# Kernel tuning notes

Measured on AMD Instinct MI355X. Metric: run time of the kernel, lower is better.

Reference implementation:

```python
import jax, jax.numpy as jnp
import numpy as np

D_MODEL = 1024
N_HEADS = 16
MIXTURE_FACTOR = 4
LATENT = D_MODEL // MIXTURE_FACTOR  # 256
D_K = D_MODEL // N_HEADS            # 64
B, L = 2, 2048


def setup_inputs() -> dict:
    key = jax.random.key(0)
    ks = jax.random.split(key, 13)
    s_in = 1.0 / np.sqrt(D_MODEL)
    s_lat = 1.0 / np.sqrt(LATENT)
    return {
        "queries": jax.random.normal(ks[0], (B, L, 1, D_MODEL), jnp.float32),
        "keys": jax.random.normal(ks[1], (B, L, 1, D_MODEL), jnp.float32),
        "values": jax.random.normal(ks[2], (B, L, 1, D_MODEL), jnp.float32),
        "Wq": jax.random.normal(ks[3], (D_MODEL, D_MODEL), jnp.float32) * s_in,
        "bq": jnp.zeros((D_MODEL,), jnp.float32),
        "Wd": jax.random.normal(ks[4], (D_MODEL, LATENT), jnp.float32) * s_in,
        "bd": jnp.zeros((LATENT,), jnp.float32),
        "Wk": jax.random.normal(ks[5], (LATENT, D_MODEL), jnp.float32) * s_lat,
        "bk": jnp.zeros((D_MODEL,), jnp.float32),
        "Wv": jax.random.normal(ks[6], (LATENT, D_MODEL), jnp.float32) * s_lat,
        "bv": jnp.zeros((D_MODEL,), jnp.float32),
        "Wo": jax.random.normal(ks[7], (D_MODEL, D_MODEL), jnp.float32) * s_in,
        "bo": jnp.zeros((D_MODEL,), jnp.float32),
    }


def reference(queries, keys, values, Wq, bq, Wd, bd, Wk, bk, Wv, bv, Wo, bo):
    b, l, h_in, e = queries.shape  # h_in == 1, e == d_model
    s = keys.shape[1]
    scale = D_K ** -0.5

    q_flat = queries.reshape(b, l, e)
    Q = (q_flat @ Wq + bq).reshape(b, l, N_HEADS, D_K)

    kv_input = keys.reshape(b, s, e)
    latent = kv_input @ Wd + bd                      # [b, s, latent]
    K = (latent @ Wk + bk).reshape(b, s, N_HEADS, D_K)
    V = (latent @ Wv + bv).reshape(b, s, N_HEADS, D_K)

    scores = jnp.einsum('blhe,bshe->bhls', Q, K) * scale  # [b, h, l, s]
    causal = jnp.triu(jnp.ones((l, s), dtype=bool), k=1)
    scores = jnp.where(causal, -jnp.inf, scores)
    A = jax.nn.softmax(scores, axis=-1)

    out = jnp.einsum('bhls,bshd->blhd', A, V).reshape(b, l, N_HEADS * D_K)
    return out @ Wo + bo
```

## Files before the change

### kernel.cpp

```cpp
#include <hip/hip_runtime.h>
#include <stdint.h>


#define DM 1024
#define NH 16
#define DK 64
#define LL 2048

typedef float  f32x4  __attribute__((ext_vector_type(4)));
typedef __bf16 bf16x8 __attribute__((ext_vector_type(8)));
typedef short  s16x8  __attribute__((ext_vector_type(8)));

__device__ __forceinline__ unsigned short f2bf(float f) {
    union { float f; unsigned int u; } v; v.f = f;
    return (unsigned short)((v.u + 0x7fffu + ((v.u >> 16) & 1u)) >> 16);
}
__device__ __forceinline__ unsigned int pack2(float a, float b) {
    return (unsigned int)f2bf(a) | ((unsigned int)f2bf(b) << 16);
}
__device__ __forceinline__ bf16x8 ld8(const unsigned short* p) {
    s16x8 s = *(const s16x8*)p;
    return __builtin_bit_cast(bf16x8, s);
}
__device__ __forceinline__ void gl16(const void* g, void* l) {
    __builtin_amdgcn_global_load_lds((__attribute__((address_space(1))) void*)(g),
                                     (__attribute__((address_space(3))) void*)(l),
                                     16, 0, 0);
}

__global__ __launch_bounds__(256)
void prep_k(const float* __restrict__ Wq, const float* __restrict__ Wd,
            const float* __restrict__ Wk, const float* __restrict__ Wv,
            const float* __restrict__ Wo, const float* __restrict__ queries,
            const float* __restrict__ keys,
            unsigned short* __restrict__ WqT, unsigned short* __restrict__ WdT,
            unsigned short* __restrict__ WkvT, unsigned short* __restrict__ WoT,
            unsigned short* __restrict__ Qb, unsigned short* __restrict__ Kb) {
    int bid = blockIdx.x;
    const int t = threadIdx.x;

    const float* W; unsigned short* WT; int TK, TN;
    if (bid < 1024)      { W = Wq; WT = WqT;  TK = 1024; TN = 1024; }
    else if (bid < 1280) { bid -= 1024; W = Wd; WT = WdT; TK = 1024; TN = 256; }
    else if (bid < 1536) { bid -= 1280; W = Wk; WT = WkvT; TK = 256; TN = 1024; }
    else if (bid < 1792) { bid -= 1536; W = Wv; WT = WkvT + (size_t)1024 * 256; TK = 256; TN = 1024; }
    else if (bid < 2816) { bid -= 1792; W = Wo; WT = WoT;  TK = 1024; TN = 1024; }
    else {
        bid -= 2816;
        const float* src; unsigned short* dst;
        if (bid < 1024) { src = queries; dst = Qb; }
        else            { bid -= 1024; src = keys; dst = Kb; }
        const size_t base = (size_t)bid * 4096;
#pragma unroll
        for (int i = 0; i < 4; ++i) {
            float4 f = *(const float4*)(src + base + (size_t)(i * 256 + t) * 4);
            uint2 u = { pack2(f.x, f.y), pack2(f.z, f.w) };
            *(uint2*)(dst + base + (size_t)(i * 256 + t) * 4) = u;
        }
        return;
    }
    __shared__ float tile[32][33];
    const int tx = t & 31, ty = t >> 5;
    const int bx = bid % (TK / 32), by = bid / (TK / 32);
    const int k0 = bx * 32, n0 = by * 32;
#pragma unroll
    for (int i = 0; i < 4; ++i)
        tile[ty + 8 * i][tx] = W[(size_t)(k0 + ty + 8 * i) * TN + n0 + tx];
    __syncthreads();
#pragma unroll
    for (int i = 0; i < 4; ++i)
        WT[(size_t)(n0 + ty + 8 * i) * TK + k0 + tx] = f2bf(tile[tx][ty + 8 * i]);
}

__device__ __forceinline__ void stage6(const unsigned short* gA, const unsigned short* gB,
                                       int kk, int K,
                                       unsigned short* lA, unsigned short* lB) {
#pragma unroll
    for (int s = 0; s < 4; ++s) gl16(gA + kk + (size_t)s * 8 * K, lA + s * 512);
#pragma unroll
    for (int s = 0; s < 2; ++s) gl16(gB + kk + (size_t)s * 8 * K, lB + s * 512);
}

__device__ __forceinline__ void mfma16(const unsigned short* As, const unsigned short* Bs,
                                       const int aoff[4][2], const int boff[2][2],
                                       f32x4 acc[4][2]) {
#pragma unroll
    for (int ks = 0; ks < 2; ++ks) {
        bf16x8 a[4], b[2];
#pragma unroll
        for (int i = 0; i < 4; ++i) a[i] = ld8(As + aoff[i][ks]);
#pragma unroll
        for (int j = 0; j < 2; ++j) b[j] = ld8(Bs + boff[j][ks]);
#pragma unroll
        for (int i = 0; i < 4; ++i)
#pragma unroll
            for (int j = 0; j < 2; ++j)
                acc[i][j] = __builtin_amdgcn_mfma_f32_16x16x32_bf16(a[i], b[j], acc[i][j], 0, 0, 0);
    }
}

template<int MODE>
__global__ __launch_bounds__(256)
void gemm_k(const unsigned short* __restrict__ Ap, const unsigned short* __restrict__ Bt,
            const float* __restrict__ bias, void* __restrict__ Cp,
            const unsigned short* __restrict__ Ap2, const unsigned short* __restrict__ Bt2,
            const float* __restrict__ bias2, void* __restrict__ Cp2,
            int K) {
    __shared__ unsigned short Sh0[12288];
    __shared__ unsigned short Sh1[12288];

    int bid = blockIdx.x;
    const unsigned short* A;
    const unsigned short* B;
    const float* bs;
    bool second = false;
    int m0, n0;
    if (MODE == 0 && bid >= 512) {
        bid -= 512; A = Ap2; B = Bt2; bs = bias2; second = true;
        const int xcd = bid & 7, s = bid >> 3;
        n0 = (s & 3) * 64; m0 = (xcd * 4 + (s >> 2)) * 128;
    } else {
        A = Ap; B = Bt; bs = bias;
        const int xcd = bid & 7, s = bid >> 3;
        if (MODE == 2) { n0 = (s & 31) * 64; m0 = (xcd * 4 + (s >> 5)) * 128; }
        else           { n0 = (s & 15) * 64; m0 = (xcd * 4 + (s >> 4)) * 128; }
    }

    const int t = threadIdx.x, lane = t & 63, wv = t >> 6;
    const int quad = lane >> 4, l15 = lane & 15;

    const int lr8 = lane >> 3;
    const int g8 = (lane & 7) ^ (lr8 & 7);
    const unsigned short* gA = A + (size_t)(m0 + wv * 32 + lr8) * K + g8 * 8;
    const unsigned short* gB = B + (size_t)(n0 + wv * 16 + lr8) * K + g8 * 8;
    unsigned short* lA0 = Sh0 + wv * 2048;
    unsigned short* lB0 = Sh0 + 8192 + wv * 1024;
    unsigned short* lA1 = Sh1 + wv * 2048;
    unsigned short* lB1 = Sh1 + 8192 + wv * 1024;

    int aoff[4][2], boff[2][2];
#pragma unroll
    for (int i = 0; i < 4; ++i) {
        const int ra = (wv >> 1) * 64 + i * 16 + l15;
#pragma unroll
        for (int ks = 0; ks < 2; ++ks)
            aoff[i][ks] = ra * 64 + (((ks * 4 + quad) ^ (ra & 7)) << 3);
    }
#pragma unroll
    for (int j = 0; j < 2; ++j) {
        const int rb = (wv & 1) * 32 + j * 16 + l15;
#pragma unroll
        for (int ks = 0; ks < 2; ++ks)
            boff[j][ks] = rb * 64 + (((ks * 4 + quad) ^ (rb & 7)) << 3);
    }

    f32x4 acc[4][2] = {};
    const int niter = K >> 6;

    stage6(gA, gB, 0, K, lA0, lB0);
    __syncthreads();
    for (int it = 0; it < niter; it += 2) {
        const int kk = it << 6;
        if (it + 1 < niter) stage6(gA, gB, kk + 64, K, lA1, lB1);
        mfma16(Sh0, Sh0 + 8192, aoff, boff, acc);
        __syncthreads();
        if (it + 1 < niter) {
            if (it + 2 < niter) stage6(gA, gB, kk + 128, K, lA0, lB0);
            mfma16(Sh1, Sh1 + 8192, aoff, boff, acc);
            __syncthreads();
        }
    }

    const bool isV = (MODE == 2) && (n0 >= 1024);
    if (!isV) {
#pragma unroll
        for (int j = 0; j < 2; ++j) {
            const int col = n0 + (wv & 1) * 32 + j * 16 + l15;
            const float bvv = bs[col];
#pragma unroll
            for (int i = 0; i < 4; ++i) {
                const int rowb = m0 + (wv >> 1) * 64 + i * 16 + quad * 4;
#pragma unroll
                for (int r = 0; r < 4; ++r) {
                    const float v = acc[i][j][r] + bvv;
                    const int row = rowb + r;
                    if (MODE == 1)
                        ((float*)Cp)[(size_t)row * 1024 + col] = v;
                    else if (second)
                        ((unsigned short*)Cp2)[(size_t)row * 256 + col] = f2bf(v);
                    else
                        ((unsigned short*)Cp)[(size_t)row * 1024 + col] = f2bf(v);
                }
            }
        }
    } else {
        unsigned short* Ld = Sh0;
#pragma unroll
        for (int j = 0; j < 2; ++j) {
            const int dloc = (wv & 1) * 32 + j * 16 + l15;
            const float bvv = bias2[(n0 - 1024) + dloc];
#pragma unroll
            for (int i = 0; i < 4; ++i) {
                const int tokb = (wv >> 1) * 64 + i * 16 + quad * 4;
#pragma unroll
                for (int r = 0; r < 4; ++r)
                    Ld[dloc * 136 + tokb + r] = f2bf(acc[i][j][r] + bvv);
            }
        }
        __syncthreads();
        const int dloc = t >> 2;
        const int tk0 = (t & 3) * 32;
        const int bb = m0 >> 11;
        unsigned short* dst = (unsigned short*)Cp2 +
            ((size_t)bb * 1024 + (n0 - 1024) + dloc) * LL + (m0 & (LL - 1)) + tk0;
        const unsigned short* srcp = Ld + dloc * 136 + tk0;
#pragma unroll
        for (int c = 0; c < 4; ++c)
            *(uint4*)(dst + c * 8) = *(const uint4*)(srcp + c * 8);
    }
}

__global__ __launch_bounds__(512)
void attn6_k(const unsigned short* __restrict__ Qp,
             const unsigned short* __restrict__ Kp,
             const unsigned short* __restrict__ VpT,
             unsigned short* __restrict__ Op) {
    __shared__ unsigned short Ks[2][4096];
    __shared__ unsigned short Vs[2][4096];
    __shared__ unsigned short Ps[8][16][72];

    const int t = threadIdx.x, lane = t & 63, wv = t >> 6;
    const int grp = wv >> 2, w4 = wv & 3;
    const int quad = lane >> 4, l15 = lane & 15;

    const int bid = blockIdx.x;
    const int xcd = bid & 7, s = bid >> 3;
    const int pair = s & 15;
    const int combo = xcd * 4 + (s >> 4);
    const int h = combo & 15, b = combo >> 4;

    const int srow = w4 * 16 + (lane >> 3);
    const int g8 = (lane & 7) ^ ((lane >> 3) & 7);
    unsigned short* lK = &Ks[grp][w4 * 1024];
    unsigned short* lV = &Vs[grp][w4 * 1024];
    const int sw = l15 & 7;
    float* cb = (float*)&Ks[0][0];

    for (int tsel = 0; tsel < 2; ++tsel) {
        const int tile = tsel ? (31 - pair) : pair;
        const int q0 = tile * 64;

        const unsigned short* qp = Qp + (size_t)(b * LL + q0 + w4 * 16 + l15) * DM + h * DK;
        const bf16x8 aq0 = ld8(qp + quad * 8);
        const bf16x8 aq1 = ld8(qp + 32 + quad * 8);

        f32x4 acc[4] = {};
        float lrow[4] = {0.f, 0.f, 0.f, 0.f};
        const int rowq = q0 + w4 * 16 + quad * 4;

        const int nit = tile / 2 + 1;
        for (int it = 0; it < nit; ++it) {
            const int c = 2 * it + grp;
            const bool active = (c <= tile);
            const int kt = c * 64;
            __syncthreads();
            if (active) {
                const unsigned short* kg = Kp + (size_t)(b * LL + kt + srow) * DM + h * DK + g8 * 8;
                const unsigned short* vg = VpT + ((size_t)(b * NH + h) * DK + srow) * LL + kt + g8 * 8;
                gl16(kg, lK);             gl16(kg + (size_t)8 * DM, lK + 512);
                gl16(vg, lV);             gl16(vg + (size_t)8 * LL, lV + 512);
            }
            __syncthreads();
            if (!active) continue;

            f32x4 s4[4];
#pragma unroll
            for (int sub = 0; sub < 4; ++sub) {
                const int base = (sub * 16 + l15) * 64;
                f32x4 ss = {};
                bf16x8 b0 = ld8(&Ks[grp][base + ((quad ^ sw) << 3)]);
                ss = __builtin_amdgcn_mfma_f32_16x16x32_bf16(aq0, b0, ss, 0, 0, 0);
                bf16x8 b1 = ld8(&Ks[grp][base + (((4 + quad) ^ sw) << 3)]);
                ss = __builtin_amdgcn_mfma_f32_16x16x32_bf16(aq1, b1, ss, 0, 0, 0);
                s4[sub] = ss;
            }

            if (c == tile) {
#pragma unroll
                for (int sub = 0; sub < 4; ++sub) {
                    const int col = kt + sub * 16 + l15;
#pragma unroll
                    for (int r = 0; r < 4; ++r) {
                        float e = exp2f(fmaf(s4[sub][r], 0.18033688011112042f, -16.0f));
                        if (col > rowq + r) e = 0.f;
                        lrow[r] += e;
                        Ps[wv][quad * 4 + r][sub * 16 + l15] =
                            (unsigned short)(__builtin_bit_cast(unsigned int, e) >> 16);
                    }
                }
            } else {
#pragma unroll
                for (int sub = 0; sub < 4; ++sub) {
#pragma unroll
                    for (int r = 0; r < 4; ++r) {
                        float e = exp2f(fmaf(s4[sub][r], 0.18033688011112042f, -16.0f));
                        lrow[r] += e;
                        Ps[wv][quad * 4 + r][sub * 16 + l15] =
                            (unsigned short)(__builtin_bit_cast(unsigned int, e) >> 16);
                    }
                }
            }

#pragma unroll
            for (int ks = 0; ks < 2; ++ks) {
                bf16x8 ap = ld8(&Ps[wv][l15][ks * 32 + quad * 8]);
#pragma unroll
                for (int sub = 0; sub < 4; ++sub) {
                    bf16x8 bv = ld8(&Vs[grp][(sub * 16 + l15) * 64 + (((ks * 4 + quad) ^ sw) << 3)]);
                    acc[sub] = __builtin_amdgcn_mfma_f32_16x16x32_bf16(ap, bv, acc[sub], 0, 0, 0);
                }
            }
        }

        __syncthreads();
        const int base = (w4 * 64 + lane) * 20;
        if (grp == 1) {
#pragma unroll
            for (int sub = 0; sub < 4; ++sub)
#pragma unroll
                for (int r = 0; r < 4; ++r) cb[base + sub * 4 + r] = acc[sub][r];
#pragma unroll
            for (int r = 0; r < 4; ++r) cb[base + 16 + r] = lrow[r];
        }
        __syncthreads();
        if (grp == 0) {
#pragma unroll
            for (int sub = 0; sub < 4; ++sub)
#pragma unroll
                for (int r = 0; r < 4; ++r) acc[sub][r] += cb[base + sub * 4 + r];
#pragma unroll
            for (int r = 0; r < 4; ++r) {
                lrow[r] += cb[base + 16 + r];
#pragma unroll
                for (int off = 1; off < 16; off <<= 1)
                    lrow[r] += __shfl_xor(lrow[r], off, 64);
                lrow[r] = __builtin_amdgcn_rcpf(lrow[r]);
            }
#pragma unroll
            for (int sub = 0; sub < 4; ++sub)
#pragma unroll
                for (int r = 0; r < 4; ++r)
                    Op[(size_t)(b * LL + rowq + r) * DM + h * DK + sub * 16 + l15] =
                        f2bf(acc[sub][r] * lrow[r]);
        }
    }
}

extern "C" void kernel_launch(void* const* d_in, const int* in_sizes, int n_in,
                              void* d_out, int out_size, void* d_ws, size_t ws_size,
                              hipStream_t stream) {
    const float* queries = (const float*)d_in[0];
    const float* keys    = (const float*)d_in[1];
    const float* Wq = (const float*)d_in[3];  const float* bq = (const float*)d_in[4];
    const float* Wd = (const float*)d_in[5];  const float* bd = (const float*)d_in[6];
    const float* Wk = (const float*)d_in[7];  const float* bk = (const float*)d_in[8];
    const float* Wv = (const float*)d_in[9];  const float* bv = (const float*)d_in[10];
    const float* Wo = (const float*)d_in[11]; const float* bo = (const float*)d_in[12];

    char* ws = (char*)d_ws;
    const size_t MB = 1048576;
    unsigned short* Qp   = (unsigned short*)(ws);
    unsigned short* Kb   = (unsigned short*)(ws + 8 * MB);
    unsigned short* Kp   = (unsigned short*)(ws + 8 * MB);
    unsigned short* Qb   = (unsigned short*)(ws + 16 * MB);
    unsigned short* VpT  = (unsigned short*)(ws + 16 * MB);
    unsigned short* WqT  = (unsigned short*)(ws + 24 * MB);
    unsigned short* Lat  = (unsigned short*)(ws + 26 * MB);
    unsigned short* WdT  = (unsigned short*)(ws + 28 * MB);
    unsigned short* WkvT = (unsigned short*)(ws + 28 * MB + 524288);
    unsigned short* Attn = (unsigned short*)(ws + 24 * MB);
    unsigned short* WoT  = (unsigned short*)(ws + 32 * MB);

    prep_k<<<4864, 256, 0, stream>>>(Wq, Wd, Wk, Wv, Wo, queries, keys,
                                     WqT, WdT, WkvT, WoT, Qb, Kb);
    gemm_k<0><<<640, 256, 0, stream>>>(Qb, WqT, bq, Qp, Kb, WdT, bd, Lat, 1024);
    gemm_k<2><<<1024, 256, 0, stream>>>(Lat, WkvT, bk, Kp, nullptr, nullptr, bv, VpT, 256);
    attn6_k<<<512, 512, 0, stream>>>(Qp, Kp, VpT, Attn);
    gemm_k<1><<<512, 256, 0, stream>>>(Attn, WoT, bo, d_out, nullptr, nullptr, nullptr, nullptr, 1024);
}
```

Before: 198.0 us.

## Read K/V directly from global memory, one query tile per block

The attention kernel no longer stages K and V tiles through LDS with global_load_lds. Each wave now loads its MFMA operands straight from global memory, with the QK^T operands swapped so the score layout fits a per-row softmax sum. The paired-tile loop is replaced by one query tile per block over twice as many blocks (largest tiles first), with an occupancy hint of 6 and truncating bf16 packing of the probabilities. This removes the LDS staging traffic and its barriers, but it relies on L1/L2 to serve repeated K/V reads and gives up the balanced pairing of short and long causal tiles.

```diff
diff --git a/kernel.cpp b/kernel.cpp
--- a/kernel.cpp
+++ b/kernel.cpp
@@ -17,6 +17,10 @@
 }
 __device__ __forceinline__ unsigned int pack2(float a, float b) {
     return (unsigned int)f2bf(a) | ((unsigned int)f2bf(b) << 16);
+}
+__device__ __forceinline__ unsigned int packt(float a, float b) {
+    union { float f; unsigned int u; } x, y; x.f = a; y.f = b;
+    return (x.u >> 16) | (y.u & 0xffff0000u);
 }
 __device__ __forceinline__ bf16x8 ld8(const unsigned short* p) {
     s16x8 s = *(const s16x8*)p;
@@ -220,14 +224,13 @@
     }
 }
 
-__global__ __launch_bounds__(512)
-void attn6_k(const unsigned short* __restrict__ Qp,
+__global__ __launch_bounds__(512, 6)
+void attn7_k(const unsigned short* __restrict__ Qp,
              const unsigned short* __restrict__ Kp,
              const unsigned short* __restrict__ VpT,
              unsigned short* __restrict__ Op) {
-    __shared__ unsigned short Ks[2][4096];
-    __shared__ unsigned short Vs[2][4096];
-    __shared__ unsigned short Ps[8][16][72];
+    __shared__ unsigned short Ps[10240];
+    float* CB = (float*)Ps;
 
     const int t = threadIdx.x, lane = t & 63, wv = t >> 6;
     const int grp = wv >> 2, w4 = wv & 3;
@@ -235,124 +238,106 @@
 
     const int bid = blockIdx.x;
     const int xcd = bid & 7, s = bid >> 3;
-    const int pair = s & 15;
-    const int combo = xcd * 4 + (s >> 4);
+    const int combo = xcd * 4 + (s & 3);
+    const int tile = 31 - (s >> 2);
     const int h = combo & 15, b = combo >> 4;
-
-    const int srow = w4 * 16 + (lane >> 3);
-    const int g8 = (lane & 7) ^ ((lane >> 3) & 7);
-    unsigned short* lK = &Ks[grp][w4 * 1024];
-    unsigned short* lV = &Vs[grp][w4 * 1024];
-    const int sw = l15 & 7;
-    float* cb = (float*)&Ks[0][0];
-
-    for (int tsel = 0; tsel < 2; ++tsel) {
-        const int tile = tsel ? (31 - pair) : pair;
-        const int q0 = tile * 64;
-
-        const unsigned short* qp = Qp + (size_t)(b * LL + q0 + w4 * 16 + l15) * DM + h * DK;
-        const bf16x8 aq0 = ld8(qp + quad * 8);
-        const bf16x8 aq1 = ld8(qp + 32 + quad * 8);
-
-        f32x4 acc[4] = {};
-        float lrow[4] = {0.f, 0.f, 0.f, 0.f};
-        const int rowq = q0 + w4 * 16 + quad * 4;
-
-        const int nit = tile / 2 + 1;
-        for (int it = 0; it < nit; ++it) {
-            const int c = 2 * it + grp;
-            const bool active = (c <= tile);
-            const int kt = c * 64;
-            __syncthreads();
-            if (active) {
-                const unsigned short* kg = Kp + (size_t)(b * LL + kt + srow) * DM + h * DK + g8 * 8;
-                const unsigned short* vg = VpT + ((size_t)(b * NH + h) * DK + srow) * LL + kt + g8 * 8;
-                gl16(kg, lK);             gl16(kg + (size_t)8 * DM, lK + 512);
-                gl16(vg, lV);             gl16(vg + (size_t)8 * LL, lV + 512);
-            }
-            __syncthreads();
-            if (!active) continue;
-
-            f32x4 s4[4];
-#pragma unroll
-            for (int sub = 0; sub < 4; ++sub) {
-                const int base = (sub * 16 + l15) * 64;
-                f32x4 ss = {};
-                bf16x8 b0 = ld8(&Ks[grp][base + ((quad ^ sw) << 3)]);
-                ss = __builtin_amdgcn_mfma_f32_16x16x32_bf16(aq0, b0, ss, 0, 0, 0);
-                bf16x8 b1 = ld8(&Ks[grp][base + (((4 + quad) ^ sw) << 3)]);
-                ss = __builtin_amdgcn_mfma_f32_16x16x32_bf16(aq1, b1, ss, 0, 0, 0);
-                s4[sub] = ss;
-            }
-
-            if (c == tile) {
-#pragma unroll
-                for (int sub = 0; sub < 4; ++sub) {
-                    const int col = kt + sub * 16 + l15;
-#pragma unroll
-                    for (int r = 0; r < 4; ++r) {
-                        float e = exp2f(fmaf(s4[sub][r], 0.18033688011112042f, -16.0f));
-                        if (col > rowq + r) e = 0.f;
-                        lrow[r] += e;
-                        Ps[wv][quad * 4 + r][sub * 16 + l15] =
-                            (unsigned short)(__builtin_bit_cast(unsigned int, e) >> 16);
-                    }
+    const int q0 = tile * 64;
+    const int rowq = q0 + w4 * 16 + l15;
+
+    const unsigned short* qp = Qp + (size_t)(b * LL + rowq) * DM + h * DK;
+    const bf16x8 aq0 = ld8(qp + quad * 8);
+    const bf16x8 aq1 = ld8(qp + 32 + quad * 8);
+
+    unsigned koff[4], voff[4];
+#pragma unroll
+    for (int sub = 0; sub < 4; ++sub) {
+        koff[sub] = (unsigned)((b * LL + sub * 16 + l15) * DM + h * DK + quad * 8);
+        voff[sub] = (unsigned)(((b * NH + h) * DK + sub * 16 + l15) * LL + quad * 8);
+    }
+
+    unsigned short* PsW = Ps + wv * 1152;
+
+    f32x4 acc[4] = {};
+    float lsum = 0.f;
+
+    const int nit = tile / 2 + 1;
+    for (int it = 0; it < nit; ++it) {
+        const int c = 2 * it + grp;
+        const bool active = (c <= tile);
+        __syncthreads();
+        if (!active) continue;
+        const int kt = c * 64;
+        const unsigned short* kb = Kp + (size_t)kt * DM;
+        const unsigned short* vb = VpT + kt;
+        const bool diag = (c == tile);
+
+#pragma unroll
+        for (int sub = 0; sub < 4; ++sub) {
+            const unsigned short* kp2 = kb + koff[sub];
+            const bf16x8 k0 = ld8(kp2);
+            const bf16x8 k1 = ld8(kp2 + 32);
+            f32x4 ss = {};
+            ss = __builtin_amdgcn_mfma_f32_16x16x32_bf16(k0, aq0, ss, 0, 0, 0);
+            ss = __builtin_amdgcn_mfma_f32_16x16x32_bf16(k1, aq1, ss, 0, 0, 0);
+            float e[4];
+            if (diag) {
+                const int kb4 = kt + sub * 16 + quad * 4;
+#pragma unroll
+                for (int r = 0; r < 4; ++r) {
+                    const float x = exp2f(fmaf(ss[r], 0.18033688011112042f, -16.0f));
+                    e[r] = (kb4 + r > rowq) ? 0.f : x;
                 }
             } else {
 #pragma unroll
-                for (int sub = 0; sub < 4; ++sub) {
-#pragma unroll
-                    for (int r = 0; r < 4; ++r) {
-                        float e = exp2f(fmaf(s4[sub][r], 0.18033688011112042f, -16.0f));
-                        lrow[r] += e;
-                        Ps[wv][quad * 4 + r][sub * 16 + l15] =
-                            (unsigned short)(__builtin_bit_cast(unsigned int, e) >> 16);
-                    }
-                }
+                for (int r = 0; r < 4; ++r)
+                    e[r] = exp2f(fmaf(ss[r], 0.18033688011112042f, -16.0f));
             }
-
-#pragma unroll
-            for (int ks = 0; ks < 2; ++ks) {
-                bf16x8 ap = ld8(&Ps[wv][l15][ks * 32 + quad * 8]);
-#pragma unroll
-                for (int sub = 0; sub < 4; ++sub) {
-                    bf16x8 bv = ld8(&Vs[grp][(sub * 16 + l15) * 64 + (((ks * 4 + quad) ^ sw) << 3)]);
-                    acc[sub] = __builtin_amdgcn_mfma_f32_16x16x32_bf16(ap, bv, acc[sub], 0, 0, 0);
-                }
+            lsum += (e[0] + e[1]) + (e[2] + e[3]);
+            uint2 w2;
+            w2.x = packt(e[0], e[1]);
+            w2.y = packt(e[2], e[3]);
+            *(uint2*)(PsW + l15 * 72 + sub * 16 + quad * 4) = w2;
+        }
+
+#pragma unroll
+        for (int ks = 0; ks < 2; ++ks) {
+            const bf16x8 ap = ld8(PsW + l15 * 72 + ks * 32 + quad * 8);
+#pragma unroll
+            for (int sub = 0; sub < 4; ++sub) {
+                const bf16x8 bv = ld8(vb + voff[sub] + ks * 32);
+                acc[sub] = __builtin_amdgcn_mfma_f32_16x16x32_bf16(ap, bv, acc[sub], 0, 0, 0);
             }
         }
-
-        __syncthreads();
-        const int base = (w4 * 64 + lane) * 20;
-        if (grp == 1) {
-#pragma unroll
-            for (int sub = 0; sub < 4; ++sub)
-#pragma unroll
-                for (int r = 0; r < 4; ++r) cb[base + sub * 4 + r] = acc[sub][r];
-#pragma unroll
-            for (int r = 0; r < 4; ++r) cb[base + 16 + r] = lrow[r];
-        }
-        __syncthreads();
-        if (grp == 0) {
-#pragma unroll
-            for (int sub = 0; sub < 4; ++sub)
-#pragma unroll
-                for (int r = 0; r < 4; ++r) acc[sub][r] += cb[base + sub * 4 + r];
-#pragma unroll
-            for (int r = 0; r < 4; ++r) {
-                lrow[r] += cb[base + 16 + r];
-#pragma unroll
-                for (int off = 1; off < 16; off <<= 1)
-                    lrow[r] += __shfl_xor(lrow[r], off, 64);
-                lrow[r] = __builtin_amdgcn_rcpf(lrow[r]);
-            }
-#pragma unroll
-            for (int sub = 0; sub < 4; ++sub)
-#pragma unroll
-                for (int r = 0; r < 4; ++r)
-                    Op[(size_t)(b * LL + rowq + r) * DM + h * DK + sub * 16 + l15] =
-                        f2bf(acc[sub][r] * lrow[r]);
-        }
+    }
+
+    __syncthreads();
+    const int base = (w4 * 64 + lane) * 20;
+    if (grp == 1) {
+#pragma unroll
+        for (int sub = 0; sub < 4; ++sub)
+#pragma unroll
+            for (int r = 0; r < 4; ++r) CB[base + sub * 4 + r] = acc[sub][r];
+        CB[base + 16] = lsum;
+    }
+    __syncthreads();
+    if (grp == 0) {
+#pragma unroll
+        for (int sub = 0; sub < 4; ++sub)
+#pragma unroll
+            for (int r = 0; r < 4; ++r) acc[sub][r] += CB[base + sub * 4 + r];
+        lsum += CB[base + 16];
+        lsum += __shfl_xor(lsum, 16, 64);
+        lsum += __shfl_xor(lsum, 32, 64);
+        const float inv = __builtin_amdgcn_rcpf(lsum);
+        float invr[4];
+#pragma unroll
+        for (int r = 0; r < 4; ++r) invr[r] = __shfl(inv, quad * 4 + r, 64);
+#pragma unroll
+        for (int sub = 0; sub < 4; ++sub)
+#pragma unroll
+            for (int r = 0; r < 4; ++r)
+                Op[(size_t)(b * LL + q0 + w4 * 16 + quad * 4 + r) * DM + h * DK + sub * 16 + l15] =
+                    f2bf(acc[sub][r] * invr[r]);
     }
 }
 
@@ -385,6 +370,6 @@
                                      WqT, WdT, WkvT, WoT, Qb, Kb);
     gemm_k<0><<<640, 256, 0, stream>>>(Qb, WqT, bq, Qp, Kb, WdT, bd, Lat, 1024);
     gemm_k<2><<<1024, 256, 0, stream>>>(Lat, WkvT, bk, Kp, nullptr, nullptr, bv, VpT, 256);
-    attn6_k<<<512, 512, 0, stream>>>(Qp, Kp, VpT, Attn);
+    attn7_k<<<1024, 512, 0, stream>>>(Qp, Kp, VpT, Attn);
     gemm_k<1><<<512, 256, 0, stream>>>(Attn, WoT, bo, d_out, nullptr, nullptr, nullptr, nullptr, 1024);
 }
```

Measured after the change: 292.7 us. 1.48x slower.
